# Kernel tuning notes

Measured on AMD Instinct MI355X. Metric: run time of the kernel, lower is better.

The kernel has to match this reference:

```python
import jax, jax.numpy as jnp
import numpy as np

D_MODEL = 1024
N_HEADS = 16
HEAD_DIM = D_MODEL // N_HEADS


def setup_inputs() -> dict:
    key = jax.random.key(0)
    ks = jax.random.split(key, 5)
    x = jax.random.normal(ks[0], (4, 2048, D_MODEL), dtype=jnp.float32)
    s = 1.0 / np.sqrt(D_MODEL)
    W_qkv = jax.random.uniform(ks[1], (D_MODEL, 3 * D_MODEL), minval=-s, maxval=s, dtype=jnp.float32)
    b_qkv = jax.random.uniform(ks[2], (3 * D_MODEL,), minval=-s, maxval=s, dtype=jnp.float32)
    W_out = jax.random.uniform(ks[3], (D_MODEL, D_MODEL), minval=-s, maxval=s, dtype=jnp.float32)
    b_out = jax.random.uniform(ks[4], (D_MODEL,), minval=-s, maxval=s, dtype=jnp.float32)
    return {"x": x, "W_qkv": W_qkv, "b_qkv": b_qkv, "W_out": W_out, "b_out": b_out}


def reference(x, W_qkv, b_qkv, W_out, b_out):
    B, S, _ = x.shape
    qkv = x @ W_qkv + b_qkv                                   # [B,S,3*D]
    qkv = qkv.reshape(B, S, 3, N_HEADS, HEAD_DIM)
    qkv = jnp.transpose(qkv, (2, 0, 3, 1, 4))                 # [3,B,H,S,Dh]
    Q, K, V = qkv[0], qkv[1], qkv[2]
    scores = jnp.einsum('bhqd,bhkd->bhqk', Q, K) / np.sqrt(HEAD_DIM)
    attn = jax.nn.softmax(scores, axis=-1)
    out = jnp.einsum('bhqk,bhkd->bhqd', attn, V)              # [B,H,S,Dh]
    out = jnp.transpose(out, (0, 2, 1, 3)).reshape(B, S, D_MODEL)
    return out @ W_out + b_out
```

## Files before the change

kernel.cpp:

```cpp
#include <hip/hip_runtime.h>
#include <stdint.h>

typedef __attribute__((ext_vector_type(8))) short short8;
typedef __attribute__((ext_vector_type(4))) float f32x4;
typedef __attribute__((ext_vector_type(16))) float f32x16;
typedef __attribute__((ext_vector_type(4))) float float4v;
typedef __attribute__((ext_vector_type(4))) unsigned short ushort4v;
typedef __attribute__((ext_vector_type(2))) unsigned int uint2v;
typedef __attribute__((ext_vector_type(4))) unsigned int uint4v;

#define MFMA16(a,b,c) __builtin_amdgcn_mfma_f32_16x16x32_bf16((a),(b),(c),0,0,0)
#define MFMA32(a,b,c) __builtin_amdgcn_mfma_f32_32x32x16_bf16((a),(b),(c),0,0,0)

typedef const __attribute__((address_space(1))) void gld_src_t;
typedef __attribute__((address_space(3))) void gld_dst_t;
#define GLOAD_LDS16(g, l) __builtin_amdgcn_global_load_lds((gld_src_t*)(g), (gld_dst_t*)(l), 16, 0, 0)

__device__ __forceinline__ unsigned short f2bf(float f) {
  union { float f; unsigned int u; } v; v.f = f;
  unsigned int u = v.u;
  unsigned int r = (u + 0x7fffu + ((u >> 16) & 1u)) >> 16;
  return (unsigned short)r;
}

__device__ __forceinline__ unsigned cvtpk(float a, float b) {
  unsigned r;
  asm("v_cvt_pk_bf16_f32 %0, %1, %2" : "=v"(r) : "v"(a), "v"(b));
  return r;
}

__device__ __forceinline__ float max3f(float a, float b, float c) {
  float d;
  asm("v_max3_f32 %0, %1, %2, %3" : "=v"(d) : "v"(a), "v"(b), "v"(c));
  return d;
}

__global__ __launch_bounds__(256) void cvt_f32_bf16(const float* __restrict__ in,
                                                    unsigned short* __restrict__ out) {
  int i = blockIdx.x * 256 + threadIdx.x;
  float4v v = ((const float4v*)in)[i];
  ushort4v o;
  o[0] = f2bf(v[0]); o[1] = f2bf(v[1]); o[2] = f2bf(v[2]); o[3] = f2bf(v[3]);
  ((ushort4v*)out)[i] = o;
}

__global__ __launch_bounds__(256) void cvt_transpose(const float* __restrict__ W,
                                                     unsigned short* __restrict__ WT,
                                                     int K, int N) {
  __shared__ unsigned short lds[64][72];
  int k0 = blockIdx.x * 64, n0 = blockIdx.y * 64;
  int t = threadIdx.x, tr = t >> 4, tc = t & 15;
#pragma unroll
  for (int p = 0; p < 4; ++p) {
    int k = tr + p * 16;
    float4v v = *(const float4v*)&W[(size_t)(k0 + k) * N + n0 + tc * 4];
    lds[tc * 4 + 0][k] = f2bf(v[0]);
    lds[tc * 4 + 1][k] = f2bf(v[1]);
    lds[tc * 4 + 2][k] = f2bf(v[2]);
    lds[tc * 4 + 3][k] = f2bf(v[3]);
  }
  __syncthreads();
#pragma unroll
  for (int p = 0; p < 4; ++p) {
    int n = tr + p * 16;
    ushort4v o;
    o[0] = lds[n][tc * 4 + 0]; o[1] = lds[n][tc * 4 + 1];
    o[2] = lds[n][tc * 4 + 2]; o[3] = lds[n][tc * 4 + 3];
    *(ushort4v*)&WT[(size_t)(n0 + n) * K + k0 + tc * 4] = o;
  }
}

__global__ __launch_bounds__(256) void transpose_v(const unsigned short* __restrict__ V,
                                                   unsigned short* __restrict__ Vt) {
  __shared__ unsigned short lds[64][72];
  int bh = blockIdx.x, s0 = blockIdx.y * 64;
  int t = threadIdx.x, tr = t >> 4, tc = t & 15;
  const unsigned short* Vb = V + (size_t)bh * 2048 * 64;
  unsigned short* Vtb = Vt + (size_t)bh * 64 * 2048;
#pragma unroll
  for (int p = 0; p < 4; ++p) {
    int s = tr + p * 16;
    ushort4v v = *(const ushort4v*)&Vb[(size_t)(s0 + s) * 64 + tc * 4];
    lds[tc * 4 + 0][s] = v[0];
    lds[tc * 4 + 1][s] = v[1];
    lds[tc * 4 + 2][s] = v[2];
    lds[tc * 4 + 3][s] = v[3];
  }
  __syncthreads();
#pragma unroll
  for (int p = 0; p < 4; ++p) {
    int d = tr + p * 16;
    ushort4v o;
    o[0] = lds[d][tc * 4 + 0]; o[1] = lds[d][tc * 4 + 1];
    o[2] = lds[d][tc * 4 + 2]; o[3] = lds[d][tc * 4 + 3];
    *(ushort4v*)&Vtb[(size_t)d * 2048 + s0 + tc * 4] = o;
  }
}

__device__ __forceinline__ void gemm_mainloop_128(const unsigned short* __restrict__ A,
                                                  const unsigned short* __restrict__ BT,
                                                  int K, int row0, int col0,
                                                  unsigned short* Als, unsigned short* Bls,
                                                  f32x4 acc[4][4]) {
  int t = threadIdx.x;
  int w = t >> 6, l = t & 63;
  int lo = l & 15, hi = l >> 4;
  int wr = w >> 1, wc = w & 1;
  const unsigned short* Ag1 = A + (size_t)(row0 + (t >> 2)) * K + (t & 3) * 8;
  const unsigned short* Ag2 = A + (size_t)(row0 + 64 + (t >> 2)) * K + (t & 3) * 8;
  const unsigned short* Bg1 = BT + (size_t)(col0 + (t >> 2)) * K + (t & 3) * 8;
  const unsigned short* Bg2 = BT + (size_t)(col0 + 64 + (t >> 2)) * K + (t & 3) * 8;
  unsigned short* Ald1 = Als + w * 512;
  unsigned short* Ald2 = Als + 2048 + w * 512;
  unsigned short* Bld1 = Bls + w * 512;
  unsigned short* Bld2 = Bls + 2048 + w * 512;
  int aoff[4], boff[4];
#pragma unroll
  for (int m = 0; m < 4; ++m) aoff[m] = (wr * 64 + m * 16 + lo) * 32 + hi * 8;
#pragma unroll
  for (int n = 0; n < 4; ++n) boff[n] = (wc * 64 + n * 16 + lo) * 32 + hi * 8;

  for (int k0 = 0; k0 < K; k0 += 32) {
    GLOAD_LDS16(Ag1 + k0, Ald1);
    GLOAD_LDS16(Ag2 + k0, Ald2);
    GLOAD_LDS16(Bg1 + k0, Bld1);
    GLOAD_LDS16(Bg2 + k0, Bld2);
    __syncthreads();
    short8 af[4], bf[4];
#pragma unroll
    for (int m = 0; m < 4; ++m) af[m] = *(const short8*)&Als[aoff[m]];
#pragma unroll
    for (int n = 0; n < 4; ++n) bf[n] = *(const short8*)&Bls[boff[n]];
#pragma unroll
    for (int m = 0; m < 4; ++m)
#pragma unroll
      for (int n = 0; n < 4; ++n)
        acc[m][n] = MFMA16(af[m], bf[n], acc[m][n]);
    __syncthreads();
  }
}

__global__ __launch_bounds__(256) void gemm_qkv(const unsigned short* __restrict__ xb,
                                                const unsigned short* __restrict__ WT,
                                                const float* __restrict__ bias,
                                                unsigned short* __restrict__ Q,
                                                unsigned short* __restrict__ Ko,
                                                unsigned short* __restrict__ V) {
  __shared__ unsigned short Als[4096], Bls[4096];
  f32x4 zero = {0.f, 0.f, 0.f, 0.f};
  f32x4 acc[4][4];
#pragma unroll
  for (int m = 0; m < 4; ++m)
#pragma unroll
    for (int n = 0; n < 4; ++n) acc[m][n] = zero;
  int row0 = blockIdx.x * 128, col0 = blockIdx.y * 128;
  gemm_mainloop_128(xb, WT, 1024, row0, col0, Als, Bls, acc);

  int t = threadIdx.x, w = t >> 6, l = t & 63, lo = l & 15, hi = l >> 4;
  int wr = w >> 1, wc = w & 1;
#pragma unroll
  for (int m = 0; m < 4; ++m) {
#pragma unroll
    for (int n = 0; n < 4; ++n) {
      int col = col0 + wc * 64 + n * 16 + lo;
      float b = bias[col];
      int which = col >> 10, hd = col & 1023, h = hd >> 6, d = hd & 63;
#pragma unroll
      for (int r = 0; r < 4; ++r) {
        int row = row0 + wr * 64 + m * 16 + hi * 4 + r;
        int bb = row >> 11, s = row & 2047;
        float v = acc[m][n][r] + b;
        size_t dst = ((size_t)(bb * 16 + h) * 2048 + s) * 64 + d;
        if (which == 0)      Q[dst]  = f2bf(v * 0.18033688011112042f);
        else if (which == 1) Ko[dst] = f2bf(v);
        else                 V[dst]  = f2bf(v);
      }
    }
  }
}

__global__ __launch_bounds__(256) void gemm_out(const unsigned short* __restrict__ attn,
                                                const unsigned short* __restrict__ WT,
                                                const float* __restrict__ bias,
                                                float* __restrict__ out) {
  __shared__ unsigned short Als[4096], Bls[4096];
  f32x4 zero = {0.f, 0.f, 0.f, 0.f};
  f32x4 acc[4][4];
#pragma unroll
  for (int m = 0; m < 4; ++m)
#pragma unroll
    for (int n = 0; n < 4; ++n) acc[m][n] = zero;
  int row0 = blockIdx.x * 128, col0 = blockIdx.y * 128;
  gemm_mainloop_128(attn, WT, 1024, row0, col0, Als, Bls, acc);

  int t = threadIdx.x, w = t >> 6, l = t & 63, lo = l & 15, hi = l >> 4;
  int wr = w >> 1, wc = w & 1;
#pragma unroll
  for (int m = 0; m < 4; ++m) {
#pragma unroll
    for (int n = 0; n < 4; ++n) {
      int col = col0 + wc * 64 + n * 16 + lo;
      float b = bias[col];
#pragma unroll
      for (int r = 0; r < 4; ++r) {
        int row = row0 + wr * 64 + m * 16 + hi * 4 + r;
        out[(size_t)row * 1024 + col] = acc[m][n][r] + b;
      }
    }
  }
}

__global__ __launch_bounds__(256, 2) void attn_fwd2(const unsigned short* __restrict__ Q,
                                                    const unsigned short* __restrict__ Kg,
                                                    const unsigned short* __restrict__ Vt,
                                                    unsigned short* __restrict__ attn_out) {
  const int S = 2048;
  __shared__ unsigned short Kls[4][4096];
  __shared__ unsigned short Vls[4][4096];

  int bid = blockIdx.x;
  int swz = (bid & 7) * 128 + (bid >> 3);
  int bh = swz >> 4, qt = swz & 15;
  int t = threadIdx.x, w = t >> 6, l = t & 63;
  int lo = l & 31, hi = l >> 5;
  int qi = qt * 128 + w * 32 + lo;
  const unsigned short* Qr = Q + ((size_t)bh * S + qi) * 64 + hi * 8;
  const char* KbB = (const char*)(Kg + (size_t)bh * S * 64);
  const char* VbB = (const char*)(Vt + (size_t)bh * 64 * S);

  short8 qf[4];
#pragma unroll
  for (int ks = 0; ks < 4; ++ks) qf[ks] = *(const short8*)(Qr + ks * 16);

  short8 onesf;
#pragma unroll
  for (int e = 0; e < 8; ++e) onesf[e] = (short)0x3F80;

  int lrow = l >> 3;
  int j0 = w * 2;
  int g0B = (((l & 7) ^ lrow ^ j0) << 4);
  int g1B = (((l & 7) ^ lrow ^ (j0 + 1)) << 4);
  size_t kg0 = (size_t)(8 * j0 + lrow) * 128 + g0B;
  size_t kg1 = (size_t)(8 * j0 + 8 + lrow) * 128 + g1B;
  size_t vg0 = (size_t)(8 * j0 + lrow) * 4096 + g0B;
  size_t vg1 = (size_t)(8 * j0 + 8 + lrow) * 4096 + g1B;

  int koff0[4], koff1[4];
#pragma unroll
  for (int ks = 0; ks < 4; ++ks) {
    int srow = (lo & 7) ^ (lo >> 3);
    koff0[ks] = lo * 64 + (((2 * ks + hi) ^ srow) << 3);
    koff1[ks] = (lo + 32) * 64 + (((2 * ks + hi) ^ srow ^ 4) << 3);
  }

#define STAGE_KV(Kd, Vd, kvoff) do {                                  \
    GLOAD_LDS16(KbB + (size_t)(kvoff) * 128 + kg0, (Kd) + j0 * 512);  \
    GLOAD_LDS16(KbB + (size_t)(kvoff) * 128 + kg1, (Kd) + (j0 + 1) * 512); \
    GLOAD_LDS16(VbB + (size_t)(kvoff) * 2 + vg0, (Vd) + j0 * 512);    \
    GLOAD_LDS16(VbB + (size_t)(kvoff) * 2 + vg1, (Vd) + (j0 + 1) * 512); \
  } while (0)

  unsigned short *Kc = &Kls[0][0], *K1 = &Kls[1][0], *K2 = &Kls[2][0], *K3 = &Kls[3][0];
  unsigned short *Vc = &Vls[0][0], *V1 = &Vls[1][0], *V2 = &Vls[2][0], *V3 = &Vls[3][0];

  STAGE_KV(Kc, Vc, 0);
  STAGE_KV(K1, V1, 64);
  STAGE_KV(K2, V2, 128);

  const f32x16 zf = {0.f,0.f,0.f,0.f,0.f,0.f,0.f,0.f,0.f,0.f,0.f,0.f,0.f,0.f,0.f,0.f};
  f32x16 ot0 = zf, ot1 = zf;
  f32x16 lacc = zf;
  float m = -1e30f;

  for (int it = 0; it < 32; ++it) {
    asm volatile("s_waitcnt vmcnt(8)" ::: "memory");
    __builtin_amdgcn_s_barrier();
    STAGE_KV(K3, V3, ((it + 3) & 31) * 64);

    short8 kf0[4], kf1[4];
#pragma unroll
    for (int ks = 0; ks < 4; ++ks) {
      kf0[ks] = *(const short8*)&Kc[koff0[ks]];
      kf1[ks] = *(const short8*)&Kc[koff1[ks]];
    }
    f32x16 st0 = zf, st1 = zf;
    __builtin_amdgcn_s_setprio(1);
#pragma unroll
    for (int ks = 0; ks < 4; ++ks) {
      st0 = MFMA32(kf0[ks], qf[ks], st0);
      st1 = MFMA32(kf1[ks], qf[ks], st1);
    }
    __builtin_amdgcn_s_setprio(0);
    short8 vf0[4], vf1[4];
#pragma unroll
    for (int ks = 0; ks < 4; ++ks) {
      vf0[ks] = *(const short8*)&Vc[koff0[ks]];
      vf1[ks] = *(const short8*)&Vc[koff1[ks]];
    }

    float a0 = max3f(st0[0], st0[1], st0[2]);
    float a1 = max3f(st0[3], st0[4], st0[5]);
    float a2 = max3f(st0[6], st0[7], st0[8]);
    float a3 = max3f(st0[9], st0[10], st0[11]);
    float a4 = max3f(st0[12], st0[13], st0[14]);
    float b0 = max3f(st1[0], st1[1], st1[2]);
    float b1 = max3f(st1[3], st1[4], st1[5]);
    float b2 = max3f(st1[6], st1[7], st1[8]);
    float b3 = max3f(st1[9], st1[10], st1[11]);
    float b4 = max3f(st1[12], st1[13], st1[14]);
    float c0 = max3f(a0, a1, a2);
    float c1 = max3f(a3, a4, st0[15]);
    float c2 = max3f(b0, b1, b2);
    float c3 = max3f(b3, b4, st1[15]);
    float pmaxh = fmaxf(max3f(c0, c1, c2), c3);
    uint2v msw = __builtin_amdgcn_permlane32_swap(__builtin_bit_cast(unsigned, pmaxh),
                                                  __builtin_bit_cast(unsigned, pmaxh),
                                                  false, false);
    float pmax = fmaxf(__builtin_bit_cast(float, msw[0]), __builtin_bit_cast(float, msw[1]));
    if (!__all(pmax - m <= 8.0f)) {
      float mnew = fmaxf(m, pmax);
      float alpha = exp2f(m - mnew);
      m = mnew;
      lacc[0] *= alpha;
#pragma unroll
      for (int r = 0; r < 16; ++r) { ot0[r] *= alpha; ot1[r] *= alpha; }
    }

    short8 pb[4];
    float p[16];
#pragma unroll
    for (int r = 0; r < 16; ++r) p[r] = exp2f(st0[r] - m);
    {
      unsigned x0 = cvtpk(p[0], p[1]),  x1 = cvtpk(p[2], p[3]);
      unsigned y0 = cvtpk(p[4], p[5]),  y1 = cvtpk(p[6], p[7]);
      uint2v sw0 = __builtin_amdgcn_permlane32_swap(x0, y0, false, false);
      uint2v sw1 = __builtin_amdgcn_permlane32_swap(x1, y1, false, false);
      uint4v pk; pk[0] = sw0[0]; pk[1] = sw1[0]; pk[2] = sw0[1]; pk[3] = sw1[1];
      pb[0] = __builtin_bit_cast(short8, pk);
      unsigned x2 = cvtpk(p[8], p[9]),  x3 = cvtpk(p[10], p[11]);
      unsigned y2 = cvtpk(p[12], p[13]), y3 = cvtpk(p[14], p[15]);
      uint2v sw2 = __builtin_amdgcn_permlane32_swap(x2, y2, false, false);
      uint2v sw3 = __builtin_amdgcn_permlane32_swap(x3, y3, false, false);
      uint4v pk1; pk1[0] = sw2[0]; pk1[1] = sw3[0]; pk1[2] = sw2[1]; pk1[3] = sw3[1];
      pb[1] = __builtin_bit_cast(short8, pk1);
    }
#pragma unroll
    for (int r = 0; r < 16; ++r) p[r] = exp2f(st1[r] - m);
    {
      unsigned x0 = cvtpk(p[0], p[1]),  x1 = cvtpk(p[2], p[3]);
      unsigned y0 = cvtpk(p[4], p[5]),  y1 = cvtpk(p[6], p[7]);
      uint2v sw0 = __builtin_amdgcn_permlane32_swap(x0, y0, false, false);
      uint2v sw1 = __builtin_amdgcn_permlane32_swap(x1, y1, false, false);
      uint4v pk; pk[0] = sw0[0]; pk[1] = sw1[0]; pk[2] = sw0[1]; pk[3] = sw1[1];
      pb[2] = __builtin_bit_cast(short8, pk);
      unsigned x2 = cvtpk(p[8], p[9]),  x3 = cvtpk(p[10], p[11]);
      unsigned y2 = cvtpk(p[12], p[13]), y3 = cvtpk(p[14], p[15]);
      uint2v sw2 = __builtin_amdgcn_permlane32_swap(x2, y2, false, false);
      uint2v sw3 = __builtin_amdgcn_permlane32_swap(x3, y3, false, false);
      uint4v pk1; pk1[0] = sw2[0]; pk1[1] = sw3[0]; pk1[2] = sw2[1]; pk1[3] = sw3[1];
      pb[3] = __builtin_bit_cast(short8, pk1);
    }

    __builtin_amdgcn_s_setprio(1);
#pragma unroll
    for (int ks = 0; ks < 4; ++ks) {
      ot0 = MFMA32(vf0[ks], pb[ks], ot0);
      ot1 = MFMA32(vf1[ks], pb[ks], ot1);
      lacc = MFMA32(onesf, pb[ks], lacc);
    }
    __builtin_amdgcn_s_setprio(0);

    unsigned short* tk = Kc; Kc = K1; K1 = K2; K2 = K3; K3 = tk;
    unsigned short* tv = Vc; Vc = V1; V1 = V2; V2 = V3; V3 = tv;
  }

  float inv = 1.0f / lacc[0];
  int b = bh >> 4, h = bh & 15;
  unsigned short* orow = attn_out + ((size_t)(b * 2048 + qi)) * 1024 + h * 64 + 4 * hi;
#pragma unroll
  for (int g = 0; g < 4; ++g) {
    uint2v u0, u1;
    u0[0] = cvtpk(ot0[4*g + 0] * inv, ot0[4*g + 1] * inv);
    u0[1] = cvtpk(ot0[4*g + 2] * inv, ot0[4*g + 3] * inv);
    u1[0] = cvtpk(ot1[4*g + 0] * inv, ot1[4*g + 1] * inv);
    u1[1] = cvtpk(ot1[4*g + 2] * inv, ot1[4*g + 3] * inv);
    *(uint2v*)(orow + 8 * g) = u0;
    *(uint2v*)(orow + 32 + 8 * g) = u1;
  }
}

extern "C" void kernel_launch(void* const* d_in, const int* in_sizes, int n_in,
                              void* d_out, int out_size, void* d_ws, size_t ws_size,
                              hipStream_t stream) {
  (void)in_sizes; (void)n_in; (void)out_size; (void)ws_size;
  const float* x     = (const float*)d_in[0];
  const float* W_qkv = (const float*)d_in[1];
  const float* b_qkv = (const float*)d_in[2];
  const float* W_out = (const float*)d_in[3];
  const float* b_out = (const float*)d_in[4];
  float* out = (float*)d_out;
  char* ws = (char*)d_ws;
  unsigned short* xb    = (unsigned short*)(ws);
  unsigned short* WqkvT = (unsigned short*)(ws + 16777216);
  unsigned short* WoutT = (unsigned short*)(ws + 23068672);
  unsigned short* Qb    = (unsigned short*)(ws + 25165824);
  unsigned short* Kb    = (unsigned short*)(ws + 41943040);
  unsigned short* Vb    = (unsigned short*)(ws + 58720256);
  unsigned short* Vtb   = (unsigned short*)(ws + 75497472);
  unsigned short* attnb = (unsigned short*)(ws + 92274688);

  cvt_f32_bf16<<<8192, 256, 0, stream>>>(x, xb);
  cvt_transpose<<<dim3(16, 48), 256, 0, stream>>>(W_qkv, WqkvT, 1024, 3072);
  cvt_transpose<<<dim3(16, 16), 256, 0, stream>>>(W_out, WoutT, 1024, 1024);
  gemm_qkv<<<dim3(64, 24), 256, 0, stream>>>(xb, WqkvT, b_qkv, Qb, Kb, Vb);
  transpose_v<<<dim3(64, 32), 256, 0, stream>>>(Vb, Vtb);
  attn_fwd2<<<1024, 256, 0, stream>>>(Qb, Kb, Vtb, attnb);
  gemm_out<<<dim3(64, 8), 256, 0, stream>>>(attnb, WoutT, b_out, out);
}
```

Baseline: 228.1 us.

## Software-pipeline QK^T with PV in attention and fuse V transpose into QKV GEMM

The attention loop is restructured so the QK^T MFMAs for the next KV tile are interleaved with the softmax and PV MFMAs of the current tile. Score accumulators ping-pong between two register sets, and the loop is unrolled by four with fixed LDS buffer indices. This is meant to hide the softmax and exp latency behind matrix-core work. Separately, the QKV GEMM epilogue writes V directly in transposed layout, which removes the transpose_v kernel launch and its extra global round trip. The costs are higher register pressure and a tighter vmcnt wait that overlaps less of the load pipeline.

```diff
diff --git a/kernel.cpp b/kernel.cpp
--- a/kernel.cpp
+++ b/kernel.cpp
@@ -67,33 +67,6 @@
     o[0] = lds[n][tc * 4 + 0]; o[1] = lds[n][tc * 4 + 1];
     o[2] = lds[n][tc * 4 + 2]; o[3] = lds[n][tc * 4 + 3];
     *(ushort4v*)&WT[(size_t)(n0 + n) * K + k0 + tc * 4] = o;
-  }
-}
-
-__global__ __launch_bounds__(256) void transpose_v(const unsigned short* __restrict__ V,
-                                                   unsigned short* __restrict__ Vt) {
-  __shared__ unsigned short lds[64][72];
-  int bh = blockIdx.x, s0 = blockIdx.y * 64;
-  int t = threadIdx.x, tr = t >> 4, tc = t & 15;
-  const unsigned short* Vb = V + (size_t)bh * 2048 * 64;
-  unsigned short* Vtb = Vt + (size_t)bh * 64 * 2048;
-#pragma unroll
-  for (int p = 0; p < 4; ++p) {
-    int s = tr + p * 16;
-    ushort4v v = *(const ushort4v*)&Vb[(size_t)(s0 + s) * 64 + tc * 4];
-    lds[tc * 4 + 0][s] = v[0];
-    lds[tc * 4 + 1][s] = v[1];
-    lds[tc * 4 + 2][s] = v[2];
-    lds[tc * 4 + 3][s] = v[3];
-  }
-  __syncthreads();
-#pragma unroll
-  for (int p = 0; p < 4; ++p) {
-    int d = tr + p * 16;
-    ushort4v o;
-    o[0] = lds[d][tc * 4 + 0]; o[1] = lds[d][tc * 4 + 1];
-    o[2] = lds[d][tc * 4 + 2]; o[3] = lds[d][tc * 4 + 3];
-    *(ushort4v*)&Vtb[(size_t)d * 2048 + s0 + tc * 4] = o;
   }
 }
 
@@ -145,7 +118,7 @@
                                                 const float* __restrict__ bias,
                                                 unsigned short* __restrict__ Q,
                                                 unsigned short* __restrict__ Ko,
-                                                unsigned short* __restrict__ V) {
+                                                unsigned short* __restrict__ Vt) {
   __shared__ unsigned short Als[4096], Bls[4096];
   f32x4 zero = {0.f, 0.f, 0.f, 0.f};
   f32x4 acc[4][4];
@@ -165,15 +138,23 @@
       int col = col0 + wc * 64 + n * 16 + lo;
       float b = bias[col];
       int which = col >> 10, hd = col & 1023, h = hd >> 6, d = hd & 63;
-#pragma unroll
-      for (int r = 0; r < 4; ++r) {
-        int row = row0 + wr * 64 + m * 16 + hi * 4 + r;
-        int bb = row >> 11, s = row & 2047;
-        float v = acc[m][n][r] + b;
-        size_t dst = ((size_t)(bb * 16 + h) * 2048 + s) * 64 + d;
-        if (which == 0)      Q[dst]  = f2bf(v * 0.18033688011112042f);
-        else if (which == 1) Ko[dst] = f2bf(v);
-        else                 V[dst]  = f2bf(v);
+      int row = row0 + wr * 64 + m * 16 + hi * 4;
+      int bb = row >> 11, s = row & 2047;
+      if (which == 2) {
+        ushort4v o;
+#pragma unroll
+        for (int r = 0; r < 4; ++r) o[r] = f2bf(acc[m][n][r] + b);
+        *(ushort4v*)&Vt[((size_t)(bb * 16 + h) * 64 + d) * 2048 + s] = o;
+      } else if (which == 0) {
+        size_t base = ((size_t)(bb * 16 + h) * 2048 + s) * 64 + d;
+#pragma unroll
+        for (int r = 0; r < 4; ++r)
+          Q[base + (size_t)r * 64] = f2bf((acc[m][n][r] + b) * 0.18033688011112042f);
+      } else {
+        size_t base = ((size_t)(bb * 16 + h) * 2048 + s) * 64 + d;
+#pragma unroll
+        for (int r = 0; r < 4; ++r)
+          Ko[base + (size_t)r * 64] = f2bf(acc[m][n][r] + b);
       }
     }
   }
@@ -260,118 +241,123 @@
     GLOAD_LDS16(VbB + (size_t)(kvoff) * 2 + vg1, (Vd) + (j0 + 1) * 512); \
   } while (0)
 
-  unsigned short *Kc = &Kls[0][0], *K1 = &Kls[1][0], *K2 = &Kls[2][0], *K3 = &Kls[3][0];
-  unsigned short *Vc = &Vls[0][0], *V1 = &Vls[1][0], *V2 = &Vls[2][0], *V3 = &Vls[3][0];
-
-  STAGE_KV(Kc, Vc, 0);
-  STAGE_KV(K1, V1, 64);
-  STAGE_KV(K2, V2, 128);
+  STAGE_KV(&Kls[0][0], &Vls[0][0], 0);
+  STAGE_KV(&Kls[1][0], &Vls[1][0], 64);
+  STAGE_KV(&Kls[2][0], &Vls[2][0], 128);
 
   const f32x16 zf = {0.f,0.f,0.f,0.f,0.f,0.f,0.f,0.f,0.f,0.f,0.f,0.f,0.f,0.f,0.f,0.f};
   f32x16 ot0 = zf, ot1 = zf;
   f32x16 lacc = zf;
   float m = -1e30f;
 
-  for (int it = 0; it < 32; ++it) {
-    asm volatile("s_waitcnt vmcnt(8)" ::: "memory");
-    __builtin_amdgcn_s_barrier();
-    STAGE_KV(K3, V3, ((it + 3) & 31) * 64);
-
+  asm volatile("s_waitcnt vmcnt(8)" ::: "memory");
+  __builtin_amdgcn_s_barrier();
+  f32x16 stA0 = zf, stA1 = zf, stB0 = zf, stB1 = zf;
+  {
     short8 kf0[4], kf1[4];
 #pragma unroll
     for (int ks = 0; ks < 4; ++ks) {
-      kf0[ks] = *(const short8*)&Kc[koff0[ks]];
-      kf1[ks] = *(const short8*)&Kc[koff1[ks]];
+      kf0[ks] = *(const short8*)&Kls[0][koff0[ks]];
+      kf1[ks] = *(const short8*)&Kls[0][koff1[ks]];
     }
-    f32x16 st0 = zf, st1 = zf;
-    __builtin_amdgcn_s_setprio(1);
 #pragma unroll
     for (int ks = 0; ks < 4; ++ks) {
-      st0 = MFMA32(kf0[ks], qf[ks], st0);
-      st1 = MFMA32(kf1[ks], qf[ks], st1);
+      stA0 = MFMA32(kf0[ks], qf[ks], stA0);
+      stA1 = MFMA32(kf1[ks], qf[ks], stA1);
     }
-    __builtin_amdgcn_s_setprio(0);
-    short8 vf0[4], vf1[4];
-#pragma unroll
-    for (int ks = 0; ks < 4; ++ks) {
-      vf0[ks] = *(const short8*)&Vc[koff0[ks]];
-      vf1[ks] = *(const short8*)&Vc[koff1[ks]];
-    }
-
-    float a0 = max3f(st0[0], st0[1], st0[2]);
-    float a1 = max3f(st0[3], st0[4], st0[5]);
-    float a2 = max3f(st0[6], st0[7], st0[8]);
-    float a3 = max3f(st0[9], st0[10], st0[11]);
-    float a4 = max3f(st0[12], st0[13], st0[14]);
-    float b0 = max3f(st1[0], st1[1], st1[2]);
-    float b1 = max3f(st1[3], st1[4], st1[5]);
-    float b2 = max3f(st1[6], st1[7], st1[8]);
-    float b3 = max3f(st1[9], st1[10], st1[11]);
-    float b4 = max3f(st1[12], st1[13], st1[14]);
-    float c0 = max3f(a0, a1, a2);
-    float c1 = max3f(a3, a4, st0[15]);
-    float c2 = max3f(b0, b1, b2);
-    float c3 = max3f(b3, b4, st1[15]);
-    float pmaxh = fmaxf(max3f(c0, c1, c2), c3);
-    uint2v msw = __builtin_amdgcn_permlane32_swap(__builtin_bit_cast(unsigned, pmaxh),
-                                                  __builtin_bit_cast(unsigned, pmaxh),
-                                                  false, false);
-    float pmax = fmaxf(__builtin_bit_cast(float, msw[0]), __builtin_bit_cast(float, msw[1]));
-    if (!__all(pmax - m <= 8.0f)) {
-      float mnew = fmaxf(m, pmax);
-      float alpha = exp2f(m - mnew);
-      m = mnew;
-      lacc[0] *= alpha;
-#pragma unroll
-      for (int r = 0; r < 16; ++r) { ot0[r] *= alpha; ot1[r] *= alpha; }
-    }
-
-    short8 pb[4];
-    float p[16];
-#pragma unroll
-    for (int r = 0; r < 16; ++r) p[r] = exp2f(st0[r] - m);
-    {
-      unsigned x0 = cvtpk(p[0], p[1]),  x1 = cvtpk(p[2], p[3]);
-      unsigned y0 = cvtpk(p[4], p[5]),  y1 = cvtpk(p[6], p[7]);
-      uint2v sw0 = __builtin_amdgcn_permlane32_swap(x0, y0, false, false);
-      uint2v sw1 = __builtin_amdgcn_permlane32_swap(x1, y1, false, false);
-      uint4v pk; pk[0] = sw0[0]; pk[1] = sw1[0]; pk[2] = sw0[1]; pk[3] = sw1[1];
-      pb[0] = __builtin_bit_cast(short8, pk);
-      unsigned x2 = cvtpk(p[8], p[9]),  x3 = cvtpk(p[10], p[11]);
-      unsigned y2 = cvtpk(p[12], p[13]), y3 = cvtpk(p[14], p[15]);
-      uint2v sw2 = __builtin_amdgcn_permlane32_swap(x2, y2, false, false);
-      uint2v sw3 = __builtin_amdgcn_permlane32_swap(x3, y3, false, false);
-      uint4v pk1; pk1[0] = sw2[0]; pk1[1] = sw3[0]; pk1[2] = sw2[1]; pk1[3] = sw3[1];
-      pb[1] = __builtin_bit_cast(short8, pk1);
-    }
-#pragma unroll
-    for (int r = 0; r < 16; ++r) p[r] = exp2f(st1[r] - m);
-    {
-      unsigned x0 = cvtpk(p[0], p[1]),  x1 = cvtpk(p[2], p[3]);
-      unsigned y0 = cvtpk(p[4], p[5]),  y1 = cvtpk(p[6], p[7]);
-      uint2v sw0 = __builtin_amdgcn_permlane32_swap(x0, y0, false, false);
-      uint2v sw1 = __builtin_amdgcn_permlane32_swap(x1, y1, false, false);
-      uint4v pk; pk[0] = sw0[0]; pk[1] = sw1[0]; pk[2] = sw0[1]; pk[3] = sw1[1];
-      pb[2] = __builtin_bit_cast(short8, pk);
-      unsigned x2 = cvtpk(p[8], p[9]),  x3 = cvtpk(p[10], p[11]);
-      unsigned y2 = cvtpk(p[12], p[13]), y3 = cvtpk(p[14], p[15]);
-      uint2v sw2 = __builtin_amdgcn_permlane32_swap(x2, y2, false, false);
-      uint2v sw3 = __builtin_amdgcn_permlane32_swap(x3, y3, false, false);
-      uint4v pk1; pk1[0] = sw2[0]; pk1[1] = sw3[0]; pk1[2] = sw2[1]; pk1[3] = sw3[1];
-      pb[3] = __builtin_bit_cast(short8, pk1);
-    }
-
-    __builtin_amdgcn_s_setprio(1);
-#pragma unroll
-    for (int ks = 0; ks < 4; ++ks) {
-      ot0 = MFMA32(vf0[ks], pb[ks], ot0);
-      ot1 = MFMA32(vf1[ks], pb[ks], ot1);
-      lacc = MFMA32(onesf, pb[ks], lacc);
-    }
-    __builtin_amdgcn_s_setprio(0);
-
-    unsigned short* tk = Kc; Kc = K1; K1 = K2; K2 = K3; K3 = tk;
-    unsigned short* tv = Vc; Vc = V1; V1 = V2; V2 = V3; V3 = tv;
+  }
+
+#define AITER(T, VB, KB, SB, SIN0, SIN1, SOUT0, SOUT1) do {                    \
+    asm volatile("s_waitcnt vmcnt(4)" ::: "memory");                           \
+    __builtin_amdgcn_s_barrier();                                              \
+    STAGE_KV(&Kls[SB][0], &Vls[SB][0], (((T) + 3) & 31) * 64);                 \
+    short8 kf0[4], kf1[4], vf0[4], vf1[4];                                     \
+    _Pragma("unroll")                                                          \
+    for (int ks = 0; ks < 4; ++ks) {                                           \
+      kf0[ks] = *(const short8*)&Kls[KB][koff0[ks]];                           \
+      kf1[ks] = *(const short8*)&Kls[KB][koff1[ks]];                           \
+      vf0[ks] = *(const short8*)&Vls[VB][koff0[ks]];                           \
+      vf1[ks] = *(const short8*)&Vls[VB][koff1[ks]];                           \
+    }                                                                          \
+    float a0 = max3f(SIN0[0], SIN0[1], SIN0[2]);                               \
+    float a1 = max3f(SIN0[3], SIN0[4], SIN0[5]);                               \
+    float a2 = max3f(SIN0[6], SIN0[7], SIN0[8]);                               \
+    float a3 = max3f(SIN0[9], SIN0[10], SIN0[11]);                             \
+    float a4 = max3f(SIN0[12], SIN0[13], SIN0[14]);                            \
+    float b0 = max3f(SIN1[0], SIN1[1], SIN1[2]);                               \
+    float b1 = max3f(SIN1[3], SIN1[4], SIN1[5]);                               \
+    float b2 = max3f(SIN1[6], SIN1[7], SIN1[8]);                               \
+    float b3 = max3f(SIN1[9], SIN1[10], SIN1[11]);                             \
+    float b4 = max3f(SIN1[12], SIN1[13], SIN1[14]);                            \
+    float c0 = max3f(a0, a1, a2);                                              \
+    float c1 = max3f(a3, a4, SIN0[15]);                                        \
+    float c2 = max3f(b0, b1, b2);                                              \
+    float c3 = max3f(b3, b4, SIN1[15]);                                        \
+    float pmaxh = fmaxf(max3f(c0, c1, c2), c3);                                \
+    uint2v msw = __builtin_amdgcn_permlane32_swap(                             \
+        __builtin_bit_cast(unsigned, pmaxh),                                   \
+        __builtin_bit_cast(unsigned, pmaxh), false, false);                    \
+    float pmax = fmaxf(__builtin_bit_cast(float, msw[0]),                      \
+                       __builtin_bit_cast(float, msw[1]));                     \
+    if (!__all(pmax - m <= 8.0f)) {                                            \
+      float mnew = fmaxf(m, pmax);                                             \
+      float alpha = exp2f(m - mnew);                                           \
+      m = mnew;                                                                \
+      lacc[0] *= alpha;                                                        \
+      _Pragma("unroll")                                                        \
+      for (int r = 0; r < 16; ++r) { ot0[r] *= alpha; ot1[r] *= alpha; }       \
+    }                                                                          \
+    short8 pb[4];                                                              \
+    {                                                                          \
+      float p[16];                                                             \
+      _Pragma("unroll")                                                        \
+      for (int r = 0; r < 16; ++r) p[r] = exp2f(SIN0[r] - m);                  \
+      unsigned x0 = cvtpk(p[0], p[1]), x1 = cvtpk(p[2], p[3]);                 \
+      unsigned y0 = cvtpk(p[4], p[5]), y1 = cvtpk(p[6], p[7]);                 \
+      uint2v sw0 = __builtin_amdgcn_permlane32_swap(x0, y0, false, false);     \
+      uint2v sw1 = __builtin_amdgcn_permlane32_swap(x1, y1, false, false);     \
+      uint4v pk; pk[0] = sw0[0]; pk[1] = sw1[0]; pk[2] = sw0[1]; pk[3] = sw1[1]; \
+      pb[0] = __builtin_bit_cast(short8, pk);                                  \
+      unsigned x2 = cvtpk(p[8], p[9]), x3 = cvtpk(p[10], p[11]);               \
+      unsigned y2 = cvtpk(p[12], p[13]), y3 = cvtpk(p[14], p[15]);             \
+      uint2v sw2 = __builtin_amdgcn_permlane32_swap(x2, y2, false, false);     \
+      uint2v sw3 = __builtin_amdgcn_permlane32_swap(x3, y3, false, false);     \
+      uint4v pk1; pk1[0] = sw2[0]; pk1[1] = sw3[0]; pk1[2] = sw2[1]; pk1[3] = sw3[1]; \
+      pb[1] = __builtin_bit_cast(short8, pk1);                                 \
+      _Pragma("unroll")                                                        \
+      for (int r = 0; r < 16; ++r) p[r] = exp2f(SIN1[r] - m);                  \
+      x0 = cvtpk(p[0], p[1]); x1 = cvtpk(p[2], p[3]);                          \
+      y0 = cvtpk(p[4], p[5]); y1 = cvtpk(p[6], p[7]);                          \
+      sw0 = __builtin_amdgcn_permlane32_swap(x0, y0, false, false);            \
+      sw1 = __builtin_amdgcn_permlane32_swap(x1, y1, false, false);            \
+      uint4v pk2; pk2[0] = sw0[0]; pk2[1] = sw1[0]; pk2[2] = sw0[1]; pk2[3] = sw1[1]; \
+      pb[2] = __builtin_bit_cast(short8, pk2);                                 \
+      x2 = cvtpk(p[8], p[9]); x3 = cvtpk(p[10], p[11]);                        \
+      y2 = cvtpk(p[12], p[13]); y3 = cvtpk(p[14], p[15]);                      \
+      sw2 = __builtin_amdgcn_permlane32_swap(x2, y2, false, false);            \
+      sw3 = __builtin_amdgcn_permlane32_swap(x3, y3, false, false);            \
+      uint4v pk3; pk3[0] = sw2[0]; pk3[1] = sw3[0]; pk3[2] = sw2[1]; pk3[3] = sw3[1]; \
+      pb[3] = __builtin_bit_cast(short8, pk3);                                 \
+    }                                                                          \
+    SOUT0 = zf; SOUT1 = zf;                                                    \
+    __builtin_amdgcn_s_setprio(1);                                             \
+    _Pragma("unroll")                                                          \
+    for (int ks = 0; ks < 4; ++ks) {                                           \
+      SOUT0 = MFMA32(kf0[ks], qf[ks], SOUT0);                                  \
+      ot0 = MFMA32(vf0[ks], pb[ks], ot0);                                      \
+      SOUT1 = MFMA32(kf1[ks], qf[ks], SOUT1);                                  \
+      ot1 = MFMA32(vf1[ks], pb[ks], ot1);                                      \
+      lacc = MFMA32(onesf, pb[ks], lacc);                                      \
+    }                                                                          \
+    __builtin_amdgcn_s_setprio(0);                                             \
+  } while (0)
+
+  for (int u = 0; u < 8; ++u) {
+    int t0 = u * 4;
+    AITER(t0 + 0, 0, 1, 3, stA0, stA1, stB0, stB1);
+    AITER(t0 + 1, 1, 2, 0, stB0, stB1, stA0, stA1);
+    AITER(t0 + 2, 2, 3, 1, stA0, stA1, stB0, stB1);
+    AITER(t0 + 3, 3, 0, 2, stB0, stB1, stA0, stA1);
   }
 
   float inv = 1.0f / lacc[0];
@@ -405,15 +391,13 @@
   unsigned short* WoutT = (unsigned short*)(ws + 23068672);
   unsigned short* Qb    = (unsigned short*)(ws + 25165824);
   unsigned short* Kb    = (unsigned short*)(ws + 41943040);
-  unsigned short* Vb    = (unsigned short*)(ws + 58720256);
   unsigned short* Vtb   = (unsigned short*)(ws + 75497472);
   unsigned short* attnb = (unsigned short*)(ws + 92274688);
 
   cvt_f32_bf16<<<8192, 256, 0, stream>>>(x, xb);
   cvt_transpose<<<dim3(16, 48), 256, 0, stream>>>(W_qkv, WqkvT, 1024, 3072);
   cvt_transpose<<<dim3(16, 16), 256, 0, stream>>>(W_out, WoutT, 1024, 1024);
-  gemm_qkv<<<dim3(64, 24), 256, 0, stream>>>(xb, WqkvT, b_qkv, Qb, Kb, Vb);
-  transpose_v<<<dim3(64, 32), 256, 0, stream>>>(Vb, Vtb);
+  gemm_qkv<<<dim3(64, 24), 256, 0, stream>>>(xb, WqkvT, b_qkv, Qb, Kb, Vtb);
   attn_fwd2<<<1024, 256, 0, stream>>>(Qb, Kb, Vtb, attnb);
   gemm_out<<<dim3(64, 8), 256, 0, stream>>>(attnb, WoutT, b_out, out);
 }
```

New measurement: 236.6 us. +3.7%, slower.

## Fuse V transpose into QKV GEMM epilogue and cut attention KV ring to three stages

Applied to the files above, without the earlier changes.

The QKV GEMM epilogue now writes V straight into the transposed [b,h,d,s] layout with 4-element vector stores, so the separate transpose_v kernel, its launch and its extra V round trip through memory go away. Separately, the attention kernel's K/V LDS ring buffer shrinks from four stages to three, with the prefetch distance and vmcnt wait adjusted to match. That lowers LDS per block, and launch bounds are raised to allow three blocks per CU. The cost is a shallower prefetch pipeline, which may expose more memory latency, plus a possible register squeeze from the tighter launch bound.

```diff
diff --git a/kernel.cpp b/kernel.cpp
--- a/kernel.cpp
+++ b/kernel.cpp
@@ -67,33 +67,6 @@
     o[0] = lds[n][tc * 4 + 0]; o[1] = lds[n][tc * 4 + 1];
     o[2] = lds[n][tc * 4 + 2]; o[3] = lds[n][tc * 4 + 3];
     *(ushort4v*)&WT[(size_t)(n0 + n) * K + k0 + tc * 4] = o;
-  }
-}
-
-__global__ __launch_bounds__(256) void transpose_v(const unsigned short* __restrict__ V,
-                                                   unsigned short* __restrict__ Vt) {
-  __shared__ unsigned short lds[64][72];
-  int bh = blockIdx.x, s0 = blockIdx.y * 64;
-  int t = threadIdx.x, tr = t >> 4, tc = t & 15;
-  const unsigned short* Vb = V + (size_t)bh * 2048 * 64;
-  unsigned short* Vtb = Vt + (size_t)bh * 64 * 2048;
-#pragma unroll
-  for (int p = 0; p < 4; ++p) {
-    int s = tr + p * 16;
-    ushort4v v = *(const ushort4v*)&Vb[(size_t)(s0 + s) * 64 + tc * 4];
-    lds[tc * 4 + 0][s] = v[0];
-    lds[tc * 4 + 1][s] = v[1];
-    lds[tc * 4 + 2][s] = v[2];
-    lds[tc * 4 + 3][s] = v[3];
-  }
-  __syncthreads();
-#pragma unroll
-  for (int p = 0; p < 4; ++p) {
-    int d = tr + p * 16;
-    ushort4v o;
-    o[0] = lds[d][tc * 4 + 0]; o[1] = lds[d][tc * 4 + 1];
-    o[2] = lds[d][tc * 4 + 2]; o[3] = lds[d][tc * 4 + 3];
-    *(ushort4v*)&Vtb[(size_t)d * 2048 + s0 + tc * 4] = o;
   }
 }
 
@@ -145,7 +118,7 @@
                                                 const float* __restrict__ bias,
                                                 unsigned short* __restrict__ Q,
                                                 unsigned short* __restrict__ Ko,
-                                                unsigned short* __restrict__ V) {
+                                                unsigned short* __restrict__ Vt) {
   __shared__ unsigned short Als[4096], Bls[4096];
   f32x4 zero = {0.f, 0.f, 0.f, 0.f};
   f32x4 acc[4][4];
@@ -165,15 +138,23 @@
       int col = col0 + wc * 64 + n * 16 + lo;
       float b = bias[col];
       int which = col >> 10, hd = col & 1023, h = hd >> 6, d = hd & 63;
-#pragma unroll
-      for (int r = 0; r < 4; ++r) {
-        int row = row0 + wr * 64 + m * 16 + hi * 4 + r;
-        int bb = row >> 11, s = row & 2047;
-        float v = acc[m][n][r] + b;
-        size_t dst = ((size_t)(bb * 16 + h) * 2048 + s) * 64 + d;
-        if (which == 0)      Q[dst]  = f2bf(v * 0.18033688011112042f);
-        else if (which == 1) Ko[dst] = f2bf(v);
-        else                 V[dst]  = f2bf(v);
+      int row = row0 + wr * 64 + m * 16 + hi * 4;
+      int bb = row >> 11, s = row & 2047;
+      if (which == 2) {
+        ushort4v o;
+#pragma unroll
+        for (int r = 0; r < 4; ++r) o[r] = f2bf(acc[m][n][r] + b);
+        *(ushort4v*)&Vt[((size_t)(bb * 16 + h) * 64 + d) * 2048 + s] = o;
+      } else if (which == 0) {
+        size_t base = ((size_t)(bb * 16 + h) * 2048 + s) * 64 + d;
+#pragma unroll
+        for (int r = 0; r < 4; ++r)
+          Q[base + (size_t)r * 64] = f2bf((acc[m][n][r] + b) * 0.18033688011112042f);
+      } else {
+        size_t base = ((size_t)(bb * 16 + h) * 2048 + s) * 64 + d;
+#pragma unroll
+        for (int r = 0; r < 4; ++r)
+          Ko[base + (size_t)r * 64] = f2bf(acc[m][n][r] + b);
       }
     }
   }
@@ -210,13 +191,13 @@
   }
 }
 
-__global__ __launch_bounds__(256, 2) void attn_fwd2(const unsigned short* __restrict__ Q,
+__global__ __launch_bounds__(256, 3) void attn_fwd2(const unsigned short* __restrict__ Q,
                                                     const unsigned short* __restrict__ Kg,
                                                     const unsigned short* __restrict__ Vt,
                                                     unsigned short* __restrict__ attn_out) {
   const int S = 2048;
-  __shared__ unsigned short Kls[4][4096];
-  __shared__ unsigned short Vls[4][4096];
+  __shared__ unsigned short Kls[3][4096];
+  __shared__ unsigned short Vls[3][4096];
 
   int bid = blockIdx.x;
   int swz = (bid & 7) * 128 + (bid >> 3);
@@ -260,12 +241,11 @@
     GLOAD_LDS16(VbB + (size_t)(kvoff) * 2 + vg1, (Vd) + (j0 + 1) * 512); \
   } while (0)
 
-  unsigned short *Kc = &Kls[0][0], *K1 = &Kls[1][0], *K2 = &Kls[2][0], *K3 = &Kls[3][0];
-  unsigned short *Vc = &Vls[0][0], *V1 = &Vls[1][0], *V2 = &Vls[2][0], *V3 = &Vls[3][0];
+  unsigned short *Kc = &Kls[0][0], *K1 = &Kls[1][0], *K2 = &Kls[2][0];
+  unsigned short *Vc = &Vls[0][0], *V1 = &Vls[1][0], *V2 = &Vls[2][0];
 
   STAGE_KV(Kc, Vc, 0);
   STAGE_KV(K1, V1, 64);
-  STAGE_KV(K2, V2, 128);
 
   const f32x16 zf = {0.f,0.f,0.f,0.f,0.f,0.f,0.f,0.f,0.f,0.f,0.f,0.f,0.f,0.f,0.f,0.f};
   f32x16 ot0 = zf, ot1 = zf;
@@ -273,9 +253,9 @@
   float m = -1e30f;
 
   for (int it = 0; it < 32; ++it) {
-    asm volatile("s_waitcnt vmcnt(8)" ::: "memory");
+    asm volatile("s_waitcnt vmcnt(4)" ::: "memory");
     __builtin_amdgcn_s_barrier();
-    STAGE_KV(K3, V3, ((it + 3) & 31) * 64);
+    STAGE_KV(K2, V2, ((it + 2) & 31) * 64);
 
     short8 kf0[4], kf1[4];
 #pragma unroll
@@ -370,8 +350,8 @@
     }
     __builtin_amdgcn_s_setprio(0);
 
-    unsigned short* tk = Kc; Kc = K1; K1 = K2; K2 = K3; K3 = tk;
-    unsigned short* tv = Vc; Vc = V1; V1 = V2; V2 = V3; V3 = tv;
+    unsigned short* tk = Kc; Kc = K1; K1 = K2; K2 = tk;
+    unsigned short* tv = Vc; Vc = V1; V1 = V2; V2 = tv;
   }
 
   float inv = 1.0f / lacc[0];
@@ -405,15 +385,13 @@
   unsigned short* WoutT = (unsigned short*)(ws + 23068672);
   unsigned short* Qb    = (unsigned short*)(ws + 25165824);
   unsigned short* Kb    = (unsigned short*)(ws + 41943040);
-  unsigned short* Vb    = (unsigned short*)(ws + 58720256);
   unsigned short* Vtb   = (unsigned short*)(ws + 75497472);
   unsigned short* attnb = (unsigned short*)(ws + 92274688);
 
   cvt_f32_bf16<<<8192, 256, 0, stream>>>(x, xb);
   cvt_transpose<<<dim3(16, 48), 256, 0, stream>>>(W_qkv, WqkvT, 1024, 3072);
   cvt_transpose<<<dim3(16, 16), 256, 0, stream>>>(W_out, WoutT, 1024, 1024);
-  gemm_qkv<<<dim3(64, 24), 256, 0, stream>>>(xb, WqkvT, b_qkv, Qb, Kb, Vb);
-  transpose_v<<<dim3(64, 32), 256, 0, stream>>>(Vb, Vtb);
+  gemm_qkv<<<dim3(64, 24), 256, 0, stream>>>(xb, WqkvT, b_qkv, Qb, Kb, Vtb);
   attn_fwd2<<<1024, 256, 0, stream>>>(Qb, Kb, Vtb, attnb);
   gemm_out<<<dim3(64, 8), 256, 0, stream>>>(attnb, WoutT, b_out, out);
 }
```

Result: no change. 230.7 us (+1.1%).
